# Optimization experiments

Measured on AMD Instinct MI355X. Metric: run time of the kernel, lower is better.

Reference implementation:

```python
import jax, jax.numpy as jnp
import numpy as np

N = 100000
DIM = 128
M = 1600000
E = 200000
HOP = 2


def setup_inputs() -> dict:
    key = jax.random.key(0)
    k1, k2, k3, k4 = jax.random.split(key, 4)
    edge = jax.random.randint(k1, (2, E), 0, N, dtype=jnp.int64)
    adj_row = jax.random.randint(k2, (M,), 0, N, dtype=jnp.int64)
    adj_col = jax.random.randint(k3, (M,), 0, N, dtype=jnp.int64)
    # degree consistent with adjacency rows (clamped to >=1 to avoid 1/0)
    deg = jax.ops.segment_sum(jnp.ones((M,), jnp.float32), adj_row, num_segments=N)
    deg = jnp.maximum(deg, 1.0).reshape(N, 1)
    # 'gaussian' signature sampling: row-L2-normalized standard normal vectors
    g = jax.random.normal(k4, (N, DIM), dtype=jnp.float32)
    x_sig = g / jnp.linalg.norm(g, axis=1, keepdims=True)
    return {"edge": edge, "adj_row": adj_row, "adj_col": adj_col, "deg": deg, "x_sig": x_sig}


def reference(edge, adj_row, adj_col, deg, x_sig):
    n = deg.shape[0]
    D = x_sig.shape[1]
    degrev = 1.0 / deg  # [N,1]
    # x: [N, 3*D] -- raw / rsqrt(deg)-scaled / rsqrt(1+log(deg))-scaled signatures
    x = jnp.concatenate(
        [x_sig, x_sig * jax.lax.rsqrt(deg), x_sig * jax.lax.rsqrt(1.0 + jnp.log(deg))],
        axis=1,
    )

    def spmm(v):  # adj_t @ v via gather + segment-sum over nnz
        return jax.ops.segment_sum(v[adj_col], adj_row, num_segments=n)

    xs = [x, degrev * spmm(x)]
    for _ in range(2, HOP + 1):
        xs.append(degrev * spmm(xs[-1]) - xs[-2])
    # [N, K, D] with K = 3*(hop+1)
    X = jnp.concatenate(xs, axis=1).reshape(n, -1, D)
    a = X[edge[0]]  # [E, K, D]
    b = X[edge[1]]  # [E, K, D]
    ret = jnp.einsum("ekd,eld->ekl", a, b)  # [E, K, K]
    ret = ret + jnp.swapaxes(ret, 1, 2)
    return ret.reshape(ret.shape[0], -1)  # [E, K*K]
```

## Files before the change

### kernel.cpp

```cpp
#include <hip/hip_runtime.h>
#include <hip/hip_fp16.h>

#define D128 128
#define X19_STRIDE 768

typedef __attribute__((ext_vector_type(8))) _Float16 f16x8;
typedef __attribute__((ext_vector_type(4))) float    f32x4;

__global__ void k_scales(const float* __restrict__ deg, float* __restrict__ scales, int N) {
  int n = blockIdx.x * blockDim.x + threadIdx.x;
  if (n >= N) return;
  float dg = deg[n];
  scales[2 * n]     = rsqrtf(dg);
  scales[2 * n + 1] = rsqrtf(1.0f + logf(dg));
}

__global__ void k_hist(const int* __restrict__ row, int* __restrict__ cnt, int M) {
  int i = blockIdx.x * blockDim.x + threadIdx.x;
  if (i < M) atomicAdd(&cnt[row[i]], 1);
}

__global__ void k_scan(const int* __restrict__ cnt, int* __restrict__ off,
                       int* __restrict__ cursor, int n) {
  __shared__ int warp_sums[16];
  int carry = 0;
  int lane = threadIdx.x & 63;
  int wid  = threadIdx.x >> 6;
  for (int base = 0; base < n; base += 1024) {
    int i = base + (int)threadIdx.x;
    int v = (i < n) ? cnt[i] : 0;
    int s = v;
    #pragma unroll
    for (int d = 1; d < 64; d <<= 1) {
      int t = __shfl_up(s, d);
      if (lane >= d) s += t;
    }
    if (lane == 63) warp_sums[wid] = s;
    __syncthreads();
    if (threadIdx.x < 16) {
      int ws = warp_sums[threadIdx.x];
      #pragma unroll
      for (int d = 1; d < 16; d <<= 1) {
        int t = __shfl_up(ws, d);
        if ((int)threadIdx.x >= d) ws += t;
      }
      warp_sums[threadIdx.x] = ws;
    }
    __syncthreads();
    int excl = (s - v) + (wid > 0 ? warp_sums[wid - 1] : 0) + carry;
    if (i < n) { off[i] = excl; cursor[i] = excl; }
    carry += warp_sums[15];
    __syncthreads();
  }
  if (threadIdx.x == 0) off[n] = carry;
}

__global__ void k_scatter(const int* __restrict__ row, const int* __restrict__ col,
                          int* __restrict__ cursor, int* __restrict__ csr_col, int M) {
  int i = blockIdx.x * blockDim.x + threadIdx.x;
  if (i < M) {
    int r = row[i];
    int pos = atomicAdd(&cursor[r], 1);
    csr_col[pos] = col[i];
  }
}

__global__ void __launch_bounds__(D128)
k_spmm1(const float* __restrict__ x_sig, const float* __restrict__ scales,
        __half* __restrict__ X19,
        const int* __restrict__ off, const int* __restrict__ csr_col,
        const float* __restrict__ deg) {
  int r = blockIdx.x;
  int d = threadIdx.x;
  __shared__ int scol[D128];
  int start = off[r], end = off[r + 1];
  float a0 = 0.f, a1 = 0.f, a2 = 0.f;
  for (int b = start; b < end; b += D128) {
    int len = min(end - b, D128);
    if (d < len) scol[d] = csr_col[b + d];
    __syncthreads();
    for (int j = 0; j < len; ++j) {
      int c = scol[j];
      float v  = x_sig[(size_t)c * D128 + d];
      float s1 = scales[2 * c];
      float s2 = scales[2 * c + 1];
      a0 += v;
      a1 += v * s1;
      a2 += v * s2;
    }
    __syncthreads();
  }
  float dr = 1.0f / deg[r];
  size_t o = (size_t)r * X19_STRIDE;
  X19[o + d]       = __float2half(a0 * dr);
  X19[o + 128 + d] = __float2half(a1 * dr);
  X19[o + 256 + d] = __float2half(a2 * dr);
}

__global__ void __launch_bounds__(192)
k_spmm2(const float* __restrict__ x_sig, const float* __restrict__ scales,
        __half* __restrict__ X19,
        const int* __restrict__ off, const int* __restrict__ csr_col,
        const float* __restrict__ deg) {
  int r = blockIdx.x;
  int t = threadIdx.x;
  __shared__ int scol[192];
  int start = off[r], end = off[r + 1];
  float acc0 = 0.f, acc1 = 0.f;
  for (int b = start; b < end; b += 192) {
    int len = min(end - b, 192);
    if (t < len) scol[t] = csr_col[b + t];
    __syncthreads();
    for (int j = 0; j < len; ++j) {
      __half2 h = *reinterpret_cast<const __half2*>(
          X19 + (size_t)scol[j] * X19_STRIDE + 2 * t);
      float2 f = __half22float2(h);
      acc0 += f.x; acc1 += f.y;
    }
    __syncthreads();
  }
  float dr = 1.0f / deg[r];
  int e0 = 2 * t;
  int k = e0 >> 7, dd = e0 & 127;
  float2 xv = *reinterpret_cast<const float2*>(x_sig + (size_t)r * D128 + dd);
  float sk = (k == 0) ? 1.0f : ((k == 1) ? scales[2 * r] : scales[2 * r + 1]);
  __half2 o;
  o.x = __float2half(acc0 * dr - xv.x * sk);
  o.y = __float2half(acc1 * dr - xv.y * sk);
  *reinterpret_cast<__half2*>(X19 + (size_t)r * X19_STRIDE + 384 + e0) = o;
}

__global__ void __launch_bounds__(256)
k_edge(const float* __restrict__ x_sig, const float* __restrict__ scales,
       const __half* __restrict__ X19, const int* __restrict__ edge,
       float* __restrict__ out, int E) {
  __shared__ float Gs[4][81];
  int w    = threadIdx.x >> 6;
  int lane = threadIdx.x & 63;
  int e = blockIdx.x * 4 + w;
  int row = lane & 15;
  int kg  = lane >> 4;

  f32x4 acc = {0.f, 0.f, 0.f, 0.f};
  if (e < E) {
    int u = edge[e];
    int v = edge[E + e];
    float su = (row == 1) ? scales[2 * u] : ((row == 2) ? scales[2 * u + 1] : 1.0f);
    float sv = (row == 1) ? scales[2 * v] : ((row == 2) ? scales[2 * v + 1] : 1.0f);
    const float*  xu = x_sig + (size_t)u * D128;
    const float*  xv = x_sig + (size_t)v * D128;
    const __half* Xu = X19 + (size_t)u * X19_STRIDE;
    const __half* Xv = X19 + (size_t)v * X19_STRIDE;
    #pragma unroll
    for (int c = 0; c < 4; ++c) {
      int koff = c * 32 + kg * 8;
      f16x8 a, b;
      if (row >= 9) {
        #pragma unroll
        for (int j = 0; j < 8; ++j) { a[j] = (_Float16)0.0f; b[j] = (_Float16)0.0f; }
      } else if (row < 3) {
        #pragma unroll
        for (int j = 0; j < 8; ++j) a[j] = (_Float16)(xu[koff + j] * su);
        #pragma unroll
        for (int j = 0; j < 8; ++j) b[j] = (_Float16)(xv[koff + j] * sv);
      } else {
        a = *reinterpret_cast<const f16x8*>(Xu + (row - 3) * D128 + koff);
        b = *reinterpret_cast<const f16x8*>(Xv + (row - 3) * D128 + koff);
      }
      acc = __builtin_amdgcn_mfma_f32_16x16x32_f16(a, b, acc, 0, 0, 0);
    }
    #pragma unroll
    for (int j = 0; j < 4; ++j) {
      int r = kg * 4 + j;
      if (r < 9 && row < 9) Gs[w][r * 9 + row] = acc[j];
    }
  }
  __syncthreads();
  if (e < E) {
    for (int t = lane; t < 81; t += 64) {
      int k = t / 9, l = t % 9;
      out[(size_t)e * 81 + t] = Gs[w][t] + Gs[w][l * 9 + k];
    }
  }
}

extern "C" void kernel_launch(void* const* d_in, const int* in_sizes, int n_in,
                              void* d_out, int out_size, void* d_ws, size_t ws_size,
                              hipStream_t stream) {
  const int*   edge    = (const int*)d_in[0];
  const int*   adj_row = (const int*)d_in[1];
  const int*   adj_col = (const int*)d_in[2];
  const float* deg     = (const float*)d_in[3];
  const float* x_sig   = (const float*)d_in[4];
  float* out = (float*)d_out;

  const int E = in_sizes[0] / 2;
  const int M = in_sizes[1];
  const int N = in_sizes[3];

  size_t x19_elems = (size_t)N * X19_STRIDE;
  size_t need = x19_elems * 2
              + (2 * (size_t)N) * 4
              + ((size_t)(N + 1) + (size_t)N + (size_t)M) * 4;
  if (ws_size < need) return;

  __half* X19   = (__half*)d_ws;
  float* scales = (float*)(X19 + x19_elems);
  int* off      = (int*)(scales + 2 * (size_t)N);
  int* cursor   = off + (N + 1);
  int* csr_col  = cursor + N;

  hipMemsetAsync(cursor, 0, (size_t)N * sizeof(int), stream);

  k_scales<<<(N + 255) / 256, 256, 0, stream>>>(deg, scales, N);
  k_hist<<<(M + 255) / 256, 256, 0, stream>>>(adj_row, cursor, M);
  k_scan<<<1, 1024, 0, stream>>>(cursor, off, cursor, N);
  k_scatter<<<(M + 255) / 256, 256, 0, stream>>>(adj_row, adj_col, cursor, csr_col, M);

  k_spmm1<<<N, D128, 0, stream>>>(x_sig, scales, X19, off, csr_col, deg);
  k_spmm2<<<N, 192, 0, stream>>>(x_sig, scales, X19, off, csr_col, deg);

  k_edge<<<(E + 3) / 4, 256, 0, stream>>>(x_sig, scales, X19, edge, out, E);
}
```

Baseline: 856.6 us.

## Parallelize CSR offset scan across blocks and vectorize edge kernel loads

Replaces the single-block serial exclusive scan over N row counts with a three-kernel block-sum / scan-of-sums / apply scheme, so the scan uses many workgroups instead of one. The edge kernel now loads all four K-chunks of operands up front, using float4 loads for the scaled raw-signature rows, before issuing the MFMA chain. This trades one long serial launch for three short ones and raises register use in the edge kernel.

```diff
diff --git a/kernel.cpp b/kernel.cpp
--- a/kernel.cpp
+++ b/kernel.cpp
@@ -20,39 +20,60 @@
   if (i < M) atomicAdd(&cnt[row[i]], 1);
 }
 
-__global__ void k_scan(const int* __restrict__ cnt, int* __restrict__ off,
-                       int* __restrict__ cursor, int n) {
+__global__ void __launch_bounds__(256)
+k_blocksum(const int* __restrict__ cnt, int* __restrict__ bsum, int n) {
+  __shared__ int ws[4];
+  int base = blockIdx.x * 1024;
+  int t = threadIdx.x;
+  int s = 0;
+  for (int j = t; j < 1024; j += 256) {
+    int i = base + j;
+    if (i < n) s += cnt[i];
+  }
+  #pragma unroll
+  for (int d = 32; d >= 1; d >>= 1) s += __shfl_down(s, d);
+  if ((t & 63) == 0) ws[t >> 6] = s;
+  __syncthreads();
+  if (t == 0) bsum[blockIdx.x] = ws[0] + ws[1] + ws[2] + ws[3];
+}
+
+__global__ void k_scan_bsums(const int* __restrict__ bsum, int* __restrict__ bpre,
+                             int* __restrict__ off, int nb, int n) {
+  if (threadIdx.x == 0 && blockIdx.x == 0) {
+    int run = 0;
+    for (int b = 0; b < nb; ++b) { bpre[b] = run; run += bsum[b]; }
+    off[n] = run;
+  }
+}
+
+__global__ void __launch_bounds__(1024)
+k_scan_apply(const int* __restrict__ cnt, const int* __restrict__ bpre,
+             int* __restrict__ off, int* __restrict__ cursor, int n) {
   __shared__ int warp_sums[16];
-  int carry = 0;
+  int i = blockIdx.x * 1024 + threadIdx.x;
   int lane = threadIdx.x & 63;
   int wid  = threadIdx.x >> 6;
-  for (int base = 0; base < n; base += 1024) {
-    int i = base + (int)threadIdx.x;
-    int v = (i < n) ? cnt[i] : 0;
-    int s = v;
+  int v = (i < n) ? cnt[i] : 0;
+  int s = v;
+  #pragma unroll
+  for (int d = 1; d < 64; d <<= 1) {
+    int t = __shfl_up(s, d);
+    if (lane >= d) s += t;
+  }
+  if (lane == 63) warp_sums[wid] = s;
+  __syncthreads();
+  if (threadIdx.x < 16) {
+    int ws = warp_sums[threadIdx.x];
     #pragma unroll
-    for (int d = 1; d < 64; d <<= 1) {
-      int t = __shfl_up(s, d);
-      if (lane >= d) s += t;
-    }
-    if (lane == 63) warp_sums[wid] = s;
-    __syncthreads();
-    if (threadIdx.x < 16) {
-      int ws = warp_sums[threadIdx.x];
-      #pragma unroll
-      for (int d = 1; d < 16; d <<= 1) {
-        int t = __shfl_up(ws, d);
-        if ((int)threadIdx.x >= d) ws += t;
-      }
-      warp_sums[threadIdx.x] = ws;
-    }
-    __syncthreads();
-    int excl = (s - v) + (wid > 0 ? warp_sums[wid - 1] : 0) + carry;
-    if (i < n) { off[i] = excl; cursor[i] = excl; }
-    carry += warp_sums[15];
-    __syncthreads();
-  }
-  if (threadIdx.x == 0) off[n] = carry;
+    for (int d = 1; d < 16; d <<= 1) {
+      int t = __shfl_up(ws, d);
+      if ((int)threadIdx.x >= d) ws += t;
+    }
+    warp_sums[threadIdx.x] = ws;
+  }
+  __syncthreads();
+  int excl = (s - v) + (wid > 0 ? warp_sums[wid - 1] : 0) + bpre[blockIdx.x];
+  if (i < n) { off[i] = excl; cursor[i] = excl; }
 }
 
 __global__ void k_scatter(const int* __restrict__ row, const int* __restrict__ col,
@@ -151,24 +172,44 @@
     const float*  xv = x_sig + (size_t)v * D128;
     const __half* Xu = X19 + (size_t)u * X19_STRIDE;
     const __half* Xv = X19 + (size_t)v * X19_STRIDE;
+
+    f16x8 a[4], b[4];
+    if (row >= 9) {
+      #pragma unroll
+      for (int c = 0; c < 4; ++c)
+        #pragma unroll
+        for (int j = 0; j < 8; ++j) { a[c][j] = (_Float16)0.0f; b[c][j] = (_Float16)0.0f; }
+    } else if (row < 3) {
+      #pragma unroll
+      for (int c = 0; c < 4; ++c) {
+        int koff = c * 32 + kg * 8;
+        float4 u0 = *reinterpret_cast<const float4*>(xu + koff);
+        float4 u1 = *reinterpret_cast<const float4*>(xu + koff + 4);
+        float4 v0 = *reinterpret_cast<const float4*>(xv + koff);
+        float4 v1 = *reinterpret_cast<const float4*>(xv + koff + 4);
+        a[c][0] = (_Float16)(u0.x * su); a[c][1] = (_Float16)(u0.y * su);
+        a[c][2] = (_Float16)(u0.z * su); a[c][3] = (_Float16)(u0.w * su);
+        a[c][4] = (_Float16)(u1.x * su); a[c][5] = (_Float16)(u1.y * su);
+        a[c][6] = (_Float16)(u1.z * su); a[c][7] = (_Float16)(u1.w * su);
+        b[c][0] = (_Float16)(v0.x * sv); b[c][1] = (_Float16)(v0.y * sv);
+        b[c][2] = (_Float16)(v0.z * sv); b[c][3] = (_Float16)(v0.w * sv);
+        b[c][4] = (_Float16)(v1.x * sv); b[c][5] = (_Float16)(v1.y * sv);
+        b[c][6] = (_Float16)(v1.z * sv); b[c][7] = (_Float16)(v1.w * sv);
+      }
+    } else {
+      const __half* pu = Xu + (row - 3) * D128;
+      const __half* pv = Xv + (row - 3) * D128;
+      #pragma unroll
+      for (int c = 0; c < 4; ++c) {
+        int koff = c * 32 + kg * 8;
+        a[c] = *reinterpret_cast<const f16x8*>(pu + koff);
+        b[c] = *reinterpret_cast<const f16x8*>(pv + koff);
+      }
+    }
     #pragma unroll
-    for (int c = 0; c < 4; ++c) {
-      int koff = c * 32 + kg * 8;
-      f16x8 a, b;
-      if (row >= 9) {
-        #pragma unroll
-        for (int j = 0; j < 8; ++j) { a[j] = (_Float16)0.0f; b[j] = (_Float16)0.0f; }
-      } else if (row < 3) {
-        #pragma unroll
-        for (int j = 0; j < 8; ++j) a[j] = (_Float16)(xu[koff + j] * su);
-        #pragma unroll
-        for (int j = 0; j < 8; ++j) b[j] = (_Float16)(xv[koff + j] * sv);
-      } else {
-        a = *reinterpret_cast<const f16x8*>(Xu + (row - 3) * D128 + koff);
-        b = *reinterpret_cast<const f16x8*>(Xv + (row - 3) * D128 + koff);
-      }
-      acc = __builtin_amdgcn_mfma_f32_16x16x32_f16(a, b, acc, 0, 0, 0);
-    }
+    for (int c = 0; c < 4; ++c)
+      acc = __builtin_amdgcn_mfma_f32_16x16x32_f16(a[c], b[c], acc, 0, 0, 0);
+
     #pragma unroll
     for (int j = 0; j < 4; ++j) {
       int r = kg * 4 + j;
@@ -197,11 +238,13 @@
   const int E = in_sizes[0] / 2;
   const int M = in_sizes[1];
   const int N = in_sizes[3];
+  const int NCHUNK = (N + 1023) / 1024;
 
   size_t x19_elems = (size_t)N * X19_STRIDE;
   size_t need = x19_elems * 2
               + (2 * (size_t)N) * 4
-              + ((size_t)(N + 1) + (size_t)N + (size_t)M) * 4;
+              + ((size_t)(N + 1) + (size_t)N + (size_t)M) * 4
+              + 2 * (size_t)NCHUNK * 4;
   if (ws_size < need) return;
 
   __half* X19   = (__half*)d_ws;
@@ -209,12 +252,16 @@
   int* off      = (int*)(scales + 2 * (size_t)N);
   int* cursor   = off + (N + 1);
   int* csr_col  = cursor + N;
+  int* bsum     = csr_col + M;
+  int* bpre     = bsum + NCHUNK;
 
   hipMemsetAsync(cursor, 0, (size_t)N * sizeof(int), stream);
 
   k_scales<<<(N + 255) / 256, 256, 0, stream>>>(deg, scales, N);
   k_hist<<<(M + 255) / 256, 256, 0, stream>>>(adj_row, cursor, M);
-  k_scan<<<1, 1024, 0, stream>>>(cursor, off, cursor, N);
+  k_blocksum<<<NCHUNK, 256, 0, stream>>>(cursor, bsum, N);
+  k_scan_bsums<<<1, 64, 0, stream>>>(bsum, bpre, off, NCHUNK, N);
+  k_scan_apply<<<NCHUNK, 1024, 0, stream>>>(cursor, bpre, off, cursor, N);
   k_scatter<<<(M + 255) / 256, 256, 0, stream>>>(adj_row, adj_col, cursor, csr_col, M);
 
   k_spmm1<<<N, D128, 0, stream>>>(x_sig, scales, X19, off, csr_col, deg);
```

Result: faster. 807.3 us (-5.8%).
